# Performance work log

Measured on AMD Instinct MI355X. Metric: run time of the kernel, lower is better.

Reference implementation:

```python
import jax, jax.numpy as jnp
import numpy as np

B, N, D, H = 4, 1024, 1024, 8
HD = D // H  # head dim = 128


def _layernorm(x, g, b, eps=1e-5):
    mu = jnp.mean(x, axis=-1, keepdims=True)
    var = jnp.mean(jnp.square(x - mu), axis=-1, keepdims=True)
    return (x - mu) * jax.lax.rsqrt(var + eps) * g + b


def setup_inputs() -> dict:
    key = jax.random.key(0)
    ks = jax.random.split(key, 8)
    x = jax.random.normal(ks[0], (B, N, D), dtype=jnp.float32)
    adj = (jax.random.uniform(ks[1], (B, N, N)) < 0.02).astype(jnp.int32)
    adj = jnp.maximum(adj, jnp.eye(N, dtype=jnp.int32)[None])  # self-loops: no empty softmax rows
    stoich = jax.random.normal(ks[2], (B, N), dtype=jnp.float32)
    s = 0.02
    W1 = jax.random.normal(ks[3], (D, 4 * D), dtype=jnp.float32) * s
    W2 = jax.random.normal(ks[4], (4 * D, D), dtype=jnp.float32) * s
    gW = jax.random.normal(ks[5], (D,), dtype=jnp.float32) * s  # Linear(1, D) weight
    return {
        "x": x, "adj_matrix": adj, "stoichiometry": stoich,
        "ln1_g": jnp.ones((D,), jnp.float32), "ln1_b": jnp.zeros((D,), jnp.float32),
        "ln2_g": jnp.ones((D,), jnp.float32), "ln2_b": jnp.zeros((D,), jnp.float32),
        "W1": W1, "b1": jnp.zeros((4 * D,), jnp.float32),
        "W2": W2, "b2": jnp.zeros((D,), jnp.float32),
        "gW": gW, "gb": jnp.zeros((D,), jnp.float32),
    }


def reference(x, adj_matrix, stoichiometry, ln1_g, ln1_b, ln2_g, ln2_b, W1, b1, W2, b2, gW, gb):
    normed = _layernorm(x, ln1_g, ln1_b)
    # q = k = v = normed, split into heads: [B, H, N, HD]
    qkv = normed.reshape(B, N, H, HD).transpose(0, 2, 1, 3)
    scores = jnp.einsum("bhqd,bhkd->bhqk", qkv, qkv) / jnp.sqrt(jnp.float32(HD))
    # stoichiometry gate: Linear(1, D) + sigmoid -> [B, N, D]; broadcast as [B, 1, N, D] (D == N)
    gates = jax.nn.sigmoid(stoichiometry[:, :, None] * gW + gb)[:, None]  # [B,1,N,N]
    mask = adj_matrix[:, None] > 0  # [B,1,N,N]
    # gate only valid entries (equivalent to (-inf)*gate since gate>0), then mask
    masked = jnp.where(mask, scores * gates, -jnp.inf)
    attn = jax.nn.softmax(masked, axis=-1)
    out = jnp.einsum("bhqk,bhkd->bhqd", attn, qkv)
    out = out.transpose(0, 2, 1, 3).reshape(B, N, D)
    x = x + out
    normed2 = _layernorm(x, ln2_g, ln2_b)
    mlp = jax.nn.gelu(normed2 @ W1 + b1, approximate=False) @ W2 + b2
    return x + mlp
```

## Files before the change

### kernel.cpp

```cpp
#include <hip/hip_runtime.h>
#include <math.h>

#define NTOK 1024
#define DMODEL 1024
#define BATCH 4

typedef __bf16 bf16x8 __attribute__((ext_vector_type(8)));
typedef float  f32x4  __attribute__((ext_vector_type(4)));
typedef unsigned short ushort_t;
typedef unsigned short us8 __attribute__((ext_vector_type(8)));

static __device__ __forceinline__ ushort_t f2bf(float f) {
  unsigned u = __float_as_uint(f);
  u += 0x7fffu + ((u >> 16) & 1u);
  return (ushort_t)(u >> 16);
}
static __device__ __forceinline__ float bf2f(ushort_t v) {
  return __uint_as_float(((unsigned)v) << 16);
}

static __device__ __forceinline__ float fast_gelu(float v) {
  const float u = 1.5957691216057308f * (v + 0.044715f * v * v * v);
  return v / (1.f + __expf(-u));
}

static __device__ __forceinline__ void gld16(void* lds, const void* g) {
  __builtin_amdgcn_global_load_lds(
      (const __attribute__((address_space(1))) void*)g,
      (__attribute__((address_space(3))) void*)lds, 16, 0, 0);
}

__global__ __launch_bounds__(256) void prep_kernel(
    const float* __restrict__ x, const float* __restrict__ g,
    const float* __restrict__ b, ushort_t* __restrict__ out,
    const float* __restrict__ W1, ushort_t* __restrict__ W1t,
    const float* __restrict__ W2, ushort_t* __restrict__ W2t)
{
  if (blockIdx.x < 4096) {
    const int row = blockIdx.x;
    const int tid = threadIdx.x;
    const float* xr = x + (size_t)row * DMODEL;
    float4 v = *(const float4*)(xr + 4 * tid);
    float s1 = v.x + v.y + v.z + v.w;
    float s2 = v.x * v.x + v.y * v.y + v.z * v.z + v.w * v.w;
#pragma unroll
    for (int d = 1; d < 64; d <<= 1) { s1 += __shfl_xor(s1, d); s2 += __shfl_xor(s2, d); }
    __shared__ float red[10];
    const int wid = tid >> 6;
    if ((tid & 63) == 0) { red[wid] = s1; red[4 + wid] = s2; }
    __syncthreads();
    if (tid == 0) {
      float a = red[0] + red[1] + red[2] + red[3];
      float c = red[4] + red[5] + red[6] + red[7];
      float mu = a / (float)DMODEL;
      float var = c / (float)DMODEL - mu * mu;
      red[8] = mu; red[9] = rsqrtf(var + 1e-5f);
    }
    __syncthreads();
    const float mu = red[8], inv = red[9];
    float4 gg = *(const float4*)(g + 4 * tid);
    float4 bb = *(const float4*)(b + 4 * tid);
    ushort4 o;
    o.x = f2bf((v.x - mu) * inv * gg.x + bb.x);
    o.y = f2bf((v.y - mu) * inv * gg.y + bb.y);
    o.z = f2bf((v.z - mu) * inv * gg.z + bb.z);
    o.w = f2bf((v.w - mu) * inv * gg.w + bb.w);
    *(ushort4*)(out + (size_t)row * DMODEL + 4 * tid) = o;
  } else {
    __shared__ float t[32][33];
    int id = blockIdx.x - 4096;
    const float* W; ushort_t* Wt; int K, N, bx, by;
    if (id < 4096) { W = W1; Wt = W1t; K = 1024; N = 4096; bx = id & 127; by = id >> 7; }
    else { id -= 4096; W = W2; Wt = W2t; K = 4096; N = 1024; bx = id & 31; by = id >> 5; }
    const int kb = by * 32, nb = bx * 32;
    const int c = threadIdx.x & 31, r0 = threadIdx.x >> 5;
#pragma unroll
    for (int r = r0; r < 32; r += 8)
      t[r][c] = W[(size_t)(kb + r) * N + nb + c];
    __syncthreads();
#pragma unroll
    for (int r = r0; r < 32; r += 8)
      Wt[(size_t)(nb + r) * K + kb + c] = f2bf(t[c][r]);
  }
}

__global__ __launch_bounds__(256) void attn_kernel(
    const float* __restrict__ x, const ushort_t* __restrict__ normedB,
    const int* __restrict__ adj, const float* __restrict__ stoich,
    const float* __restrict__ gW, const float* __restrict__ gb,
    const float* __restrict__ ln2g, const float* __restrict__ ln2b,
    const float* __restrict__ b2,
    float* __restrict__ outbase, ushort_t* __restrict__ normed2)
{
  __shared__ int   neigh[2][NTOK];
  __shared__ float gateS[2][NTOK];
  __shared__ int   cntS[2];
  __shared__ float red[2][6];

  const int tid = threadIdx.x;
  const int sub = tid >> 7;
  const int t   = tid & 127;
  const int row = blockIdx.x * 2 + sub;
  const int b   = row >> 10;

  if (tid < 2) cntS[tid] = 0;
  __syncthreads();
  const int* arow = adj + (size_t)row * NTOK;
  {
    int4 a4 = ((const int4*)arow)[t];
    int k0 = 4 * t;
    if (a4.x > 0) { int p = atomicAdd(&cntS[sub], 1); neigh[sub][p] = k0; }
    if (a4.y > 0) { int p = atomicAdd(&cntS[sub], 1); neigh[sub][p] = k0 + 1; }
    if (a4.z > 0) { int p = atomicAdd(&cntS[sub], 1); neigh[sub][p] = k0 + 2; }
    if (a4.w > 0) { int p = atomicAdd(&cntS[sub], 1); neigh[sub][p] = k0 + 3; }
    a4 = ((const int4*)arow)[t + 128];
    k0 = 4 * (t + 128);
    if (a4.x > 0) { int p = atomicAdd(&cntS[sub], 1); neigh[sub][p] = k0; }
    if (a4.y > 0) { int p = atomicAdd(&cntS[sub], 1); neigh[sub][p] = k0 + 1; }
    if (a4.z > 0) { int p = atomicAdd(&cntS[sub], 1); neigh[sub][p] = k0 + 2; }
    if (a4.w > 0) { int p = atomicAdd(&cntS[sub], 1); neigh[sub][p] = k0 + 3; }
  }
  __syncthreads();
  const int cnt = cntS[sub];

  const float st = stoich[row];
  for (int i = t; i < cnt; i += 128) {
    int k = neigh[sub][i];
    gateS[sub][i] = 1.f / (1.f + __expf(-fmaf(st, gW[k], gb[k])));
  }
  __syncthreads();

  const ushort_t* nbB = normedB + (size_t)b * NTOK * DMODEL;
  const int d0 = 8 * t;
  us8 qu = *(const us8*)(nbB + (size_t)(row & 1023) * DMODEL + d0);
  float qv[8];
#pragma unroll
  for (int j = 0; j < 8; ++j) qv[j] = bf2f(qu[j]);
  const float scale = 0.08838834764831845f;

  float lsum = 0.f;
  float o[8] = {0.f, 0.f, 0.f, 0.f, 0.f, 0.f, 0.f, 0.f};

  for (int i0 = 0; i0 < cnt; i0 += 8) {
    us8 ku[8]; float w8[8];
#pragma unroll
    for (int u = 0; u < 8; ++u) {
      const int i = i0 + u;
      const int ii = (i < cnt) ? i : 0;
      ku[u] = *(const us8*)(nbB + (size_t)neigh[sub][ii] * DMODEL + d0);
      w8[u] = gateS[sub][ii];
    }
#pragma unroll
    for (int u = 0; u < 8; ++u) {
      float p = 0.f;
#pragma unroll
      for (int j = 0; j < 8; ++j) p = fmaf(bf2f(ku[u][j]), qv[j], p);
      p += __shfl_xor(p, 1); p += __shfl_xor(p, 2);
      p += __shfl_xor(p, 4); p += __shfl_xor(p, 8);
      w8[u] *= p * scale;
    }
#pragma unroll
    for (int u = 0; u < 8; ++u)
      w8[u] = (i0 + u < cnt) ? __expf(w8[u]) : 0.f;
#pragma unroll
    for (int u = 0; u < 8; ++u) {
      lsum += w8[u];
#pragma unroll
      for (int j = 0; j < 8; ++j) o[j] = fmaf(w8[u], bf2f(ku[u][j]), o[j]);
    }
  }
  const float pinv = 1.f / lsum;

  const float* xr = x + (size_t)row * DMODEL + d0;
  const float4 xa = *(const float4*)(xr);
  const float4 xb = *(const float4*)(xr + 4);
  float r[8];
  r[0] = xa.x + o[0] * pinv; r[1] = xa.y + o[1] * pinv;
  r[2] = xa.z + o[2] * pinv; r[3] = xa.w + o[3] * pinv;
  r[4] = xb.x + o[4] * pinv; r[5] = xb.y + o[5] * pinv;
  r[6] = xb.z + o[6] * pinv; r[7] = xb.w + o[7] * pinv;

  const float4 ba = *(const float4*)(b2 + d0);
  const float4 bbv = *(const float4*)(b2 + d0 + 4);
  float4 oa, ob;
  oa.x = r[0] + ba.x;  oa.y = r[1] + ba.y;  oa.z = r[2] + ba.z;  oa.w = r[3] + ba.w;
  ob.x = r[4] + bbv.x; ob.y = r[5] + bbv.y; ob.z = r[6] + bbv.z; ob.w = r[7] + bbv.w;
  float* obp = outbase + (size_t)row * DMODEL + d0;
  *(float4*)(obp) = oa;
  *(float4*)(obp + 4) = ob;

  float s1 = 0.f, s2 = 0.f;
#pragma unroll
  for (int j = 0; j < 8; ++j) { s1 += r[j]; s2 += r[j] * r[j]; }
#pragma unroll
  for (int d = 1; d < 64; d <<= 1) { s1 += __shfl_xor(s1, d); s2 += __shfl_xor(s2, d); }
  const int wsub = (tid >> 6) & 1;
  if ((tid & 63) == 0) { red[sub][wsub] = s1; red[sub][2 + wsub] = s2; }
  __syncthreads();
  if ((tid & 127) == 0) {
    float a = red[sub][0] + red[sub][1];
    float c = red[sub][2] + red[sub][3];
    float mu = a / (float)DMODEL;
    float var = c / (float)DMODEL - mu * mu;
    red[sub][4] = mu; red[sub][5] = rsqrtf(var + 1e-5f);
  }
  __syncthreads();
  const float mu = red[sub][4], inv = red[sub][5];
  const float4 ga = *(const float4*)(ln2g + d0);
  const float4 gbv = *(const float4*)(ln2g + d0 + 4);
  const float4 la = *(const float4*)(ln2b + d0);
  const float4 lb = *(const float4*)(ln2b + d0 + 4);
  const float gg[8] = {ga.x, ga.y, ga.z, ga.w, gbv.x, gbv.y, gbv.z, gbv.w};
  const float ll[8] = {la.x, la.y, la.z, la.w, lb.x, lb.y, lb.z, lb.w};
  us8 pk;
#pragma unroll
  for (int j = 0; j < 8; ++j) pk[j] = f2bf((r[j] - mu) * inv * gg[j] + ll[j]);
  *(us8*)(normed2 + (size_t)row * DMODEL + d0) = pk;
}

__global__ __launch_bounds__(512, 2) void gemm1_pipe(
    const ushort_t* __restrict__ A, const ushort_t* __restrict__ Bt,
    const float* __restrict__ bias, ushort_t* __restrict__ Cout,
    int M, int N, int K)
{
  __shared__ __align__(16) ushort_t As[2][256 * 64];
  __shared__ __align__(16) ushort_t Bs[2][256 * 64];

  const int id = blockIdx.x;
  const int xcd = id & 7, slot = id >> 3;
  const int bm = (xcd * 2 + (slot >> 4)) * 256;
  const int bn = (slot & 15) * 256;

  const int tid = threadIdx.x;
  const int l = tid & 63;
  const int wid = tid >> 6;
  const int wrow = (wid >> 2) * 128;
  const int wcol = (wid & 3) * 64;

  const int sr = tid >> 3;
  const int sg = tid & 7;
  const int gsrc = ((sg ^ (sr & 7)) << 3);
  const ushort_t* Ag = A  + (size_t)(bm + sr) * K + gsrc;
  const ushort_t* Bg = Bt + (size_t)(bn + sr) * K + gsrc;
  const int dst = tid * 8;

  const int quad = l >> 4, lrow = l & 15;
  const int swz = lrow & 7;
  const int gx0 = ((quad ^ swz) << 3);
  const int gx1 = (((quad + 4) ^ swz) << 3);

  f32x4 acc[8][4] = {};
  bf16x8 bfr[4];

#define STAGE2(buf, kb, c0, MAT, PTR)                                          \
  gld16(&MAT[buf][(c0) * 4096 + dst],       PTR + (size_t)(c0) * 64 * K + (kb)); \
  gld16(&MAT[buf][((c0) + 1) * 4096 + dst], PTR + (size_t)((c0) + 1) * 64 * K + (kb));

#define QUARTER(buf, GX, IH, LB)                                               \
  {                                                                            \
    if (LB) {                                                                  \
      _Pragma("unroll")                                                        \
      for (int j = 0; j < 4; ++j) {                                            \
        const int rb = wcol + j * 16 + lrow;                                   \
        bfr[j] = *(const bf16x8*)(&Bs[buf][rb * 64 + (GX)]);                   \
      }                                                                        \
    }                                                                          \
    bf16x8 af[4];                                                              \
    _Pragma("unroll")                                                          \
    for (int ii = 0; ii < 4; ++ii) {                                           \
      const int ra = wrow + (IH) * 64 + ii * 16 + lrow;                        \
      af[ii] = *(const bf16x8*)(&As[buf][ra * 64 + (GX)]);                     \
    }                                                                          \
    __builtin_amdgcn_s_setprio(1);                                             \
    _Pragma("unroll")                                                          \
    for (int ii = 0; ii < 4; ++ii)                                             \
      _Pragma("unroll")                                                        \
      for (int j = 0; j < 4; ++j)                                              \
        acc[(IH) * 4 + ii][j] = __builtin_amdgcn_mfma_f32_16x16x32_bf16(       \
            af[ii], bfr[j], acc[(IH) * 4 + ii][j], 0, 0, 0);                   \
    __builtin_amdgcn_s_setprio(0);                                             \
  }

  STAGE2(0, 0, 0, As, Ag); STAGE2(0, 0, 2, As, Ag);
  STAGE2(0, 0, 0, Bs, Bg); STAGE2(0, 0, 2, Bs, Bg);
  asm volatile("s_waitcnt vmcnt(0)" ::: "memory");
  __builtin_amdgcn_s_barrier();

  const int NTK = K >> 6;
#pragma unroll 1
  for (int t = 0; t < NTK - 1; ++t) {
    const int cb = t & 1, nb = cb ^ 1;
    const int kb = (t + 1) << 6;
    STAGE2(nb, kb, 0, As, Ag);
    __builtin_amdgcn_sched_barrier(0);
    asm volatile("s_waitcnt vmcnt(2)" ::: "memory");
    __builtin_amdgcn_s_barrier();
    __builtin_amdgcn_sched_barrier(0);
    QUARTER(cb, gx0, 0, 1);
    __builtin_amdgcn_s_barrier();
    STAGE2(nb, kb, 2, As, Ag);
    QUARTER(cb, gx0, 1, 0);
    __builtin_amdgcn_s_barrier();
    STAGE2(nb, kb, 0, Bs, Bg);
    QUARTER(cb, gx1, 0, 1);
    __builtin_amdgcn_s_barrier();
    STAGE2(nb, kb, 2, Bs, Bg);
    QUARTER(cb, gx1, 1, 0);
    __builtin_amdgcn_s_barrier();
  }
  {
    const int cb = (NTK - 1) & 1;
    asm volatile("s_waitcnt vmcnt(0)" ::: "memory");
    __builtin_amdgcn_s_barrier();
    __builtin_amdgcn_sched_barrier(0);
    QUARTER(cb, gx0, 0, 1);
    QUARTER(cb, gx0, 1, 0);
    QUARTER(cb, gx1, 0, 1);
    QUARTER(cb, gx1, 1, 0);
  }
#undef STAGE2
#undef QUARTER

#pragma unroll
  for (int i = 0; i < 8; ++i) {
    const int row0 = bm + wrow + 16 * i + quad * 4;
#pragma unroll
    for (int j = 0; j < 4; ++j) {
      const int col = bn + wcol + 16 * j + lrow;
      const float bi = bias[col];
#pragma unroll
      for (int r = 0; r < 4; ++r)
        Cout[(size_t)(row0 + r) * N + col] = f2bf(fast_gelu(acc[i][j][r] + bi));
    }
  }
}

__global__ __launch_bounds__(256) void gemm_mfma_splitk(
    const ushort_t* __restrict__ A, const ushort_t* __restrict__ Bt,
    float* __restrict__ Cout, int M, int N, int K, int kchunk)
{
  __shared__ __align__(16) ushort_t As[2][128 * 32];
  __shared__ __align__(16) ushort_t Bs[2][128 * 32];

  const int id = blockIdx.x;
  const int xcd = id & 7, slot = id >> 3;
  const int bm = (xcd * 4 + (slot & 3)) * 128;
  const int bn = ((slot >> 2) & 7) * 128;
  const int koff = (slot >> 5) * kchunk;

  const int tid = threadIdx.x;
  const int w = tid >> 6, l = tid & 63;
  const int wm = (w >> 1) * 64, wn = (w & 1) * 64;

  const int srow = tid >> 2;
  const int kelem = (tid & 3) * 8;
  const ushort_t* Ag0 = A + (size_t)(bm + srow) * K + koff + kelem;
  const ushort_t* Ag1 = A + (size_t)(bm + srow + 64) * K + koff + kelem;
  const ushort_t* Bg0 = Bt + (size_t)(bn + srow) * K + koff + kelem;
  const ushort_t* Bg1 = Bt + (size_t)(bn + srow + 64) * K + koff + kelem;
  const int wb = w * 512;

  const int quad = l >> 4, lrow = l & 15;

  f32x4 acc[4][4] = {};

  for (int kb = 0; kb < kchunk; kb += 64) {
    __syncthreads();
    gld16(&As[0][wb],        Ag0 + kb);
    gld16(&As[0][wb + 2048], Ag1 + kb);
    gld16(&Bs[0][wb],        Bg0 + kb);
    gld16(&Bs[0][wb + 2048], Bg1 + kb);
    gld16(&As[1][wb],        Ag0 + kb + 32);
    gld16(&As[1][wb + 2048], Ag1 + kb + 32);
    gld16(&Bs[1][wb],        Bg0 + kb + 32);
    gld16(&Bs[1][wb + 2048], Bg1 + kb + 32);
    __syncthreads();
#pragma unroll
    for (int s = 0; s < 2; ++s) {
      const ushort_t* aRd = &As[s][(wm + lrow) * 32 + quad * 8];
      const ushort_t* bRd = &Bs[s][(wn + lrow) * 32 + quad * 8];
      bf16x8 af[4], bfr[4];
#pragma unroll
      for (int i = 0; i < 4; ++i) af[i] = *(const bf16x8*)(aRd + i * 512);
#pragma unroll
      for (int j = 0; j < 4; ++j) bfr[j] = *(const bf16x8*)(bRd + j * 512);
#pragma unroll
      for (int i = 0; i < 4; ++i)
#pragma unroll
        for (int j = 0; j < 4; ++j)
          acc[i][j] = __builtin_amdgcn_mfma_f32_16x16x32_bf16(af[i], bfr[j], acc[i][j], 0, 0, 0);
    }
  }

#pragma unroll
  for (int i = 0; i < 4; ++i) {
    const int row0 = bm + wm + 16 * i + quad * 4;
#pragma unroll
    for (int j = 0; j < 4; ++j) {
      const int col = bn + wn + 16 * j + lrow;
#pragma unroll
      for (int r = 0; r < 4; ++r) {
        const int row = row0 + r;
        atomicAdd(&Cout[(size_t)row * N + col], acc[i][j][r]);
      }
    }
  }
}

extern "C" void kernel_launch(void* const* d_in, const int* in_sizes, int n_in,
                              void* d_out, int out_size, void* d_ws, size_t ws_size,
                              hipStream_t stream) {
  const float* x      = (const float*)d_in[0];
  const int*   adj    = (const int*)d_in[1];
  const float* stoich = (const float*)d_in[2];
  const float* ln1g   = (const float*)d_in[3];
  const float* ln1b   = (const float*)d_in[4];
  const float* ln2g   = (const float*)d_in[5];
  const float* ln2b   = (const float*)d_in[6];
  const float* W1     = (const float*)d_in[7];
  const float* b1     = (const float*)d_in[8];
  const float* W2     = (const float*)d_in[9];
  const float* b2     = (const float*)d_in[10];
  const float* gW     = (const float*)d_in[11];
  const float* gb     = (const float*)d_in[12];
  float* out = (float*)d_out;
  char* ws = (char*)d_ws;

  ushort_t* normedB = (ushort_t*)(ws);
  ushort_t* normed2 = (ushort_t*)(ws + (16u << 20));
  ushort_t* hidden  = (ushort_t*)(ws + (24u << 20));
  ushort_t* W1t     = (ushort_t*)(ws + (56u << 20));
  ushort_t* W2t     = (ushort_t*)(ws + (64u << 20));

  const int ROWS = BATCH * NTOK;

  prep_kernel<<<12288, 256, 0, stream>>>(x, ln1g, ln1b, normedB,
                                         W1, W1t, W2, W2t);
  attn_kernel<<<ROWS / 2, 256, 0, stream>>>(x, normedB, adj, stoich, gW, gb,
                                            ln2g, ln2b, b2, out, normed2);
  gemm1_pipe<<<256, 512, 0, stream>>>(normed2, W1t, b1, hidden,
                                      ROWS, 4096, 1024);
  gemm_mfma_splitk<<<512, 256, 0, stream>>>(hidden, W2t, out,
                                            ROWS, 1024, 4096, 2048);
}
```

Measured before the change: 276.1 us.

## Double-buffer split-K GEMM2 with swizzled LDS and simplify GEMM1 staging

GEMM1's staging is simplified: instead of four quarter-staged loads separated by barriers, all eight next-tile loads are issued at the start of each k-step, followed by one wait and barrier. The split-K second GEMM is rewritten to match that pattern: it gets 64-wide double-buffered LDS tiles with XOR swizzling and prefetch of the next tile during the MFMAs, replacing its two-syncthreads synchronous loop. This is meant to hide global load latency and cut LDS bank conflicts and barriers. The trade-off is more LDS per block (64KB), which may limit occupancy, and the coarser GEMM1 overlap may hurt.

```diff
diff --git a/kernel.cpp b/kernel.cpp
--- a/kernel.cpp
+++ b/kernel.cpp
@@ -252,9 +252,15 @@
   f32x4 acc[8][4] = {};
   bf16x8 bfr[4];
 
-#define STAGE2(buf, kb, c0, MAT, PTR)                                          \
-  gld16(&MAT[buf][(c0) * 4096 + dst],       PTR + (size_t)(c0) * 64 * K + (kb)); \
-  gld16(&MAT[buf][((c0) + 1) * 4096 + dst], PTR + (size_t)((c0) + 1) * 64 * K + (kb));
+#define STAGE8(buf, kb)                                                        \
+  gld16(&As[buf][0 * 4096 + dst], Ag + (size_t)0 * 64 * K + (kb));             \
+  gld16(&As[buf][1 * 4096 + dst], Ag + (size_t)1 * 64 * K + (kb));             \
+  gld16(&As[buf][2 * 4096 + dst], Ag + (size_t)2 * 64 * K + (kb));             \
+  gld16(&As[buf][3 * 4096 + dst], Ag + (size_t)3 * 64 * K + (kb));             \
+  gld16(&Bs[buf][0 * 4096 + dst], Bg + (size_t)0 * 64 * K + (kb));             \
+  gld16(&Bs[buf][1 * 4096 + dst], Bg + (size_t)1 * 64 * K + (kb));             \
+  gld16(&Bs[buf][2 * 4096 + dst], Bg + (size_t)2 * 64 * K + (kb));             \
+  gld16(&Bs[buf][3 * 4096 + dst], Bg + (size_t)3 * 64 * K + (kb));
 
 #define QUARTER(buf, GX, IH, LB)                                               \
   {                                                                            \
@@ -281,44 +287,33 @@
     __builtin_amdgcn_s_setprio(0);                                             \
   }
 
-  STAGE2(0, 0, 0, As, Ag); STAGE2(0, 0, 2, As, Ag);
-  STAGE2(0, 0, 0, Bs, Bg); STAGE2(0, 0, 2, Bs, Bg);
-  asm volatile("s_waitcnt vmcnt(0)" ::: "memory");
-  __builtin_amdgcn_s_barrier();
+  STAGE8(0, 0);
 
   const int NTK = K >> 6;
 #pragma unroll 1
   for (int t = 0; t < NTK - 1; ++t) {
     const int cb = t & 1, nb = cb ^ 1;
-    const int kb = (t + 1) << 6;
-    STAGE2(nb, kb, 0, As, Ag);
-    __builtin_amdgcn_sched_barrier(0);
-    asm volatile("s_waitcnt vmcnt(2)" ::: "memory");
-    __builtin_amdgcn_s_barrier();
-    __builtin_amdgcn_sched_barrier(0);
-    QUARTER(cb, gx0, 0, 1);
-    __builtin_amdgcn_s_barrier();
-    STAGE2(nb, kb, 2, As, Ag);
-    QUARTER(cb, gx0, 1, 0);
-    __builtin_amdgcn_s_barrier();
-    STAGE2(nb, kb, 0, Bs, Bg);
-    QUARTER(cb, gx1, 0, 1);
-    __builtin_amdgcn_s_barrier();
-    STAGE2(nb, kb, 2, Bs, Bg);
-    QUARTER(cb, gx1, 1, 0);
-    __builtin_amdgcn_s_barrier();
-  }
-  {
-    const int cb = (NTK - 1) & 1;
-    asm volatile("s_waitcnt vmcnt(0)" ::: "memory");
+    STAGE8(nb, (t + 1) << 6);
+    asm volatile("s_waitcnt vmcnt(8)" ::: "memory");
     __builtin_amdgcn_s_barrier();
     __builtin_amdgcn_sched_barrier(0);
     QUARTER(cb, gx0, 0, 1);
     QUARTER(cb, gx0, 1, 0);
     QUARTER(cb, gx1, 0, 1);
     QUARTER(cb, gx1, 1, 0);
-  }
-#undef STAGE2
+    __builtin_amdgcn_s_barrier();
+  }
+  {
+    const int cb = (NTK - 1) & 1;
+    asm volatile("s_waitcnt vmcnt(0)" ::: "memory");
+    __builtin_amdgcn_s_barrier();
+    __builtin_amdgcn_sched_barrier(0);
+    QUARTER(cb, gx0, 0, 1);
+    QUARTER(cb, gx0, 1, 0);
+    QUARTER(cb, gx1, 0, 1);
+    QUARTER(cb, gx1, 1, 0);
+  }
+#undef STAGE8
 #undef QUARTER
 
 #pragma unroll
@@ -335,12 +330,12 @@
   }
 }
 
-__global__ __launch_bounds__(256) void gemm_mfma_splitk(
+__global__ __launch_bounds__(256, 2) void gemm2_pipe(
     const ushort_t* __restrict__ A, const ushort_t* __restrict__ Bt,
     float* __restrict__ Cout, int M, int N, int K, int kchunk)
 {
-  __shared__ __align__(16) ushort_t As[2][128 * 32];
-  __shared__ __align__(16) ushort_t Bs[2][128 * 32];
+  __shared__ __align__(16) ushort_t As[2][128 * 64];
+  __shared__ __align__(16) ushort_t Bs[2][128 * 64];
 
   const int id = blockIdx.x;
   const int xcd = id & 7, slot = id >> 3;
@@ -349,48 +344,77 @@
   const int koff = (slot >> 5) * kchunk;
 
   const int tid = threadIdx.x;
-  const int w = tid >> 6, l = tid & 63;
-  const int wm = (w >> 1) * 64, wn = (w & 1) * 64;
-
-  const int srow = tid >> 2;
-  const int kelem = (tid & 3) * 8;
-  const ushort_t* Ag0 = A + (size_t)(bm + srow) * K + koff + kelem;
-  const ushort_t* Ag1 = A + (size_t)(bm + srow + 64) * K + koff + kelem;
-  const ushort_t* Bg0 = Bt + (size_t)(bn + srow) * K + koff + kelem;
-  const ushort_t* Bg1 = Bt + (size_t)(bn + srow + 64) * K + koff + kelem;
-  const int wb = w * 512;
+  const int l = tid & 63;
+  const int wid = tid >> 6;
+  const int wm = (wid >> 1) * 64, wn = (wid & 1) * 64;
+
+  const int sr = tid >> 3;
+  const int sg = tid & 7;
+  const int gsrc = ((sg ^ (sr & 7)) << 3);
+  const ushort_t* Ag = A  + (size_t)(bm + sr) * K + koff + gsrc;
+  const ushort_t* Bg = Bt + (size_t)(bn + sr) * K + koff + gsrc;
+  const int dst = tid * 8;
 
   const int quad = l >> 4, lrow = l & 15;
+  const int swz = lrow & 7;
+  const int gx0 = ((quad ^ swz) << 3);
+  const int gx1 = (((quad + 4) ^ swz) << 3);
 
   f32x4 acc[4][4] = {};
 
-  for (int kb = 0; kb < kchunk; kb += 64) {
-    __syncthreads();
-    gld16(&As[0][wb],        Ag0 + kb);
-    gld16(&As[0][wb + 2048], Ag1 + kb);
-    gld16(&Bs[0][wb],        Bg0 + kb);
-    gld16(&Bs[0][wb + 2048], Bg1 + kb);
-    gld16(&As[1][wb],        Ag0 + kb + 32);
-    gld16(&As[1][wb + 2048], Ag1 + kb + 32);
-    gld16(&Bs[1][wb],        Bg0 + kb + 32);
-    gld16(&Bs[1][wb + 2048], Bg1 + kb + 32);
-    __syncthreads();
-#pragma unroll
-    for (int s = 0; s < 2; ++s) {
-      const ushort_t* aRd = &As[s][(wm + lrow) * 32 + quad * 8];
-      const ushort_t* bRd = &Bs[s][(wn + lrow) * 32 + quad * 8];
-      bf16x8 af[4], bfr[4];
-#pragma unroll
-      for (int i = 0; i < 4; ++i) af[i] = *(const bf16x8*)(aRd + i * 512);
-#pragma unroll
-      for (int j = 0; j < 4; ++j) bfr[j] = *(const bf16x8*)(bRd + j * 512);
-#pragma unroll
-      for (int i = 0; i < 4; ++i)
-#pragma unroll
-        for (int j = 0; j < 4; ++j)
-          acc[i][j] = __builtin_amdgcn_mfma_f32_16x16x32_bf16(af[i], bfr[j], acc[i][j], 0, 0, 0);
-    }
-  }
+#define STAGE8K(buf, kb)                                                       \
+  gld16(&As[buf][0 * 2048 + dst], Ag + (size_t)0 * 32 * K + (kb));             \
+  gld16(&As[buf][1 * 2048 + dst], Ag + (size_t)1 * 32 * K + (kb));             \
+  gld16(&As[buf][2 * 2048 + dst], Ag + (size_t)2 * 32 * K + (kb));             \
+  gld16(&As[buf][3 * 2048 + dst], Ag + (size_t)3 * 32 * K + (kb));             \
+  gld16(&Bs[buf][0 * 2048 + dst], Bg + (size_t)0 * 32 * K + (kb));             \
+  gld16(&Bs[buf][1 * 2048 + dst], Bg + (size_t)1 * 32 * K + (kb));             \
+  gld16(&Bs[buf][2 * 2048 + dst], Bg + (size_t)2 * 32 * K + (kb));             \
+  gld16(&Bs[buf][3 * 2048 + dst], Bg + (size_t)3 * 32 * K + (kb));
+
+#define HALF(buf, GX)                                                          \
+  {                                                                            \
+    bf16x8 af[4], bfv[4];                                                      \
+    _Pragma("unroll")                                                          \
+    for (int i = 0; i < 4; ++i)                                                \
+      af[i] = *(const bf16x8*)(&As[buf][(wm + i * 16 + lrow) * 64 + (GX)]);    \
+    _Pragma("unroll")                                                          \
+    for (int j = 0; j < 4; ++j)                                                \
+      bfv[j] = *(const bf16x8*)(&Bs[buf][(wn + j * 16 + lrow) * 64 + (GX)]);   \
+    __builtin_amdgcn_s_setprio(1);                                             \
+    _Pragma("unroll")                                                          \
+    for (int i = 0; i < 4; ++i)                                                \
+      _Pragma("unroll")                                                        \
+      for (int j = 0; j < 4; ++j)                                              \
+        acc[i][j] = __builtin_amdgcn_mfma_f32_16x16x32_bf16(                   \
+            af[i], bfv[j], acc[i][j], 0, 0, 0);                                \
+    __builtin_amdgcn_s_setprio(0);                                             \
+  }
+
+  STAGE8K(0, 0);
+
+  const int NTK = kchunk >> 6;
+#pragma unroll 1
+  for (int t = 0; t < NTK - 1; ++t) {
+    const int cb = t & 1, nb = cb ^ 1;
+    STAGE8K(nb, (t + 1) << 6);
+    asm volatile("s_waitcnt vmcnt(8)" ::: "memory");
+    __builtin_amdgcn_s_barrier();
+    __builtin_amdgcn_sched_barrier(0);
+    HALF(cb, gx0);
+    HALF(cb, gx1);
+    __builtin_amdgcn_s_barrier();
+  }
+  {
+    const int cb = (NTK - 1) & 1;
+    asm volatile("s_waitcnt vmcnt(0)" ::: "memory");
+    __builtin_amdgcn_s_barrier();
+    __builtin_amdgcn_sched_barrier(0);
+    HALF(cb, gx0);
+    HALF(cb, gx1);
+  }
+#undef STAGE8K
+#undef HALF
 
 #pragma unroll
   for (int i = 0; i < 4; ++i) {
@@ -399,10 +423,8 @@
     for (int j = 0; j < 4; ++j) {
       const int col = bn + wn + 16 * j + lrow;
 #pragma unroll
-      for (int r = 0; r < 4; ++r) {
-        const int row = row0 + r;
-        atomicAdd(&Cout[(size_t)row * N + col], acc[i][j][r]);
-      }
+      for (int r = 0; r < 4; ++r)
+        atomicAdd(&Cout[(size_t)(row0 + r) * N + col], acc[i][j][r]);
     }
   }
 }
@@ -440,6 +462,6 @@
                                             ln2g, ln2b, b2, out, normed2);
   gemm1_pipe<<<256, 512, 0, stream>>>(normed2, W1t, b1, hidden,
                                       ROWS, 4096, 1024);
-  gemm_mfma_splitk<<<512, 256, 0, stream>>>(hidden, W2t, out,
-                                            ROWS, 1024, 4096, 2048);
-}
+  gemm2_pipe<<<512, 256, 0, stream>>>(hidden, W2t, out,
+                                      ROWS, 1024, 4096, 2048);
+}
```

Result: faster. 259.3 us (-6.1%).
